# Performance work log

Measured on AMD Instinct MI355X. Metric: run time of the kernel, lower is better.

## Reference

```python
import jax, jax.numpy as jnp
import numpy as np

B, SQ, SKV, D = 4, 2048, 2048, 1024
HEADS, DIM_HEAD = 16, 64
SCALE = DIM_HEAD ** -0.5


def setup_inputs() -> dict:
    key = jax.random.key(0)
    ks = jax.random.split(key, 7)
    s = 0.02  # keep pre-softmax logits in a sane range
    return {
        "hidden_states": jax.random.normal(ks[0], (B, SQ, D), dtype=jnp.float32),
        "encoder_hidden_states": jax.random.normal(ks[1], (B, SKV, D), dtype=jnp.float32),
        "Wq": jax.random.normal(ks[2], (D, D), dtype=jnp.float32) * s,
        "Wk": jax.random.normal(ks[3], (D, D), dtype=jnp.float32) * s,
        "Wv": jax.random.normal(ks[4], (D, D), dtype=jnp.float32) * s,
        "Wo": jax.random.normal(ks[5], (D, D), dtype=jnp.float32) * s,
        "bo": jnp.zeros((D,), dtype=jnp.float32),
    }


def reference(hidden_states, encoder_hidden_states, Wq, Wk, Wv, Wo, bo):
    # to_q / to_k / to_v (bias=False)
    q = hidden_states @ Wq                       # [B, SQ, H*Dh]
    k = encoder_hidden_states @ Wk               # [B, SKV, H*Dh]
    v = encoder_hidden_states @ Wv
    # head split: [B, S, H, Dh]
    q = q.reshape(B, SQ, HEADS, DIM_HEAD)
    k = k.reshape(B, SKV, HEADS, DIM_HEAD)
    v = v.reshape(B, SKV, HEADS, DIM_HEAD)
    # scaled QK^T (baddbmm with beta=0, alpha=scale), softmax over keys
    scores = jnp.einsum("bqhd,bkhd->bhqk", q, k) * SCALE  # [B, H, SQ, SKV]
    probs = jax.nn.softmax(scores, axis=-1)
    # attention-weighted values, merge heads
    out = jnp.einsum("bhqk,bkhd->bqhd", probs, v).reshape(B, SQ, HEADS * DIM_HEAD)
    # to_out[0] linear (with bias); to_out[1] Dropout(0.0) is identity
    return out @ Wo + bo
```

## Files before the change

kernel.cpp:

```cpp
#include <hip/hip_runtime.h>

#define BATCH 4
#define SQ 2048
#define SKV 2048
#define DMODEL 1024
#define HEADS 16
#define DH 64

typedef __bf16 bf8_t __attribute__((ext_vector_type(8)));
typedef float f4_t __attribute__((ext_vector_type(4)));
typedef float f16_t __attribute__((ext_vector_type(16)));
typedef unsigned int u32;
typedef unsigned short ush;

static __device__ __forceinline__ ush f2bf(float f) {
  __bf16 h = (__bf16)f;
  return __builtin_bit_cast(ush, h);
}
static __device__ __forceinline__ u32 pk2(float a, float b) {
  return (u32)f2bf(a) | ((u32)f2bf(b) << 16);
}
static __device__ __forceinline__ void async16(const ush* g, ush* l) {
  __builtin_amdgcn_global_load_lds((const __attribute__((address_space(1))) unsigned int*)g,
                                   (__attribute__((address_space(3))) unsigned int*)l, 16, 0, 0);
}
static __device__ __forceinline__ void barrier_f() {
  asm volatile("" ::: "memory");
  __builtin_amdgcn_s_barrier();
  asm volatile("" ::: "memory");
}

__global__ __launch_bounds__(256) void prep_k(const float* __restrict__ hs,
                                              const float* __restrict__ ehs,
                                              const float* __restrict__ W0,
                                              const float* __restrict__ W1,
                                              const float* __restrict__ W2,
                                              const float* __restrict__ W3,
                                              ush* __restrict__ wT,
                                              ush* __restrict__ hsb, ush* __restrict__ ehsb) {
  __shared__ ush t[64][72];
  const int bx = blockIdx.x;
  const int tid = threadIdx.x;
  if (bx < 8192) {
    const float* X = bx < 4096 ? hs : ehs;
    ush* Y = bx < 4096 ? hsb : ehsb;
    const size_t i = ((size_t)(bx & 4095) * 256 + tid) * 8;
    float4 a = *reinterpret_cast<const float4*>(X + i);
    float4 b = *reinterpret_cast<const float4*>(X + i + 4);
    uint4 u = {pk2(a.x, a.y), pk2(a.z, a.w), pk2(b.x, b.y), pk2(b.z, b.w)};
    *reinterpret_cast<uint4*>(Y + i) = u;
    return;
  }
  const int idx = bx - 8192;
  const int z = idx >> 8, kb = (idx >> 4) & 15, nb = idx & 15;
  const float* W = z == 0 ? W0 : z == 1 ? W1 : z == 2 ? W2 : W3;
  const float scl = (z == 0) ? 0.125f * 1.44269504088896f : 1.0f;
  ush* o = wT + (size_t)z * (DMODEL * DMODEL);
  const int k0 = kb * 64, n0 = nb * 64;
#pragma unroll
  for (int it = 0; it < 4; ++it) {
    int c = tid + it * 256;
    int r = c >> 4, q4 = c & 15;
    float4 v = *reinterpret_cast<const float4*>(&W[(size_t)(k0 + r) * DMODEL + n0 + q4 * 4]);
    t[q4 * 4 + 0][r] = f2bf(v.x * scl);
    t[q4 * 4 + 1][r] = f2bf(v.y * scl);
    t[q4 * 4 + 2][r] = f2bf(v.z * scl);
    t[q4 * 4 + 3][r] = f2bf(v.w * scl);
  }
  __syncthreads();
#pragma unroll
  for (int it = 0; it < 2; ++it) {
    int c = tid + it * 256;
    int r = c >> 3, s8 = c & 7;
    uint4 pv;
    pv.x = (u32)t[r][s8 * 8 + 0] | ((u32)t[r][s8 * 8 + 1] << 16);
    pv.y = (u32)t[r][s8 * 8 + 2] | ((u32)t[r][s8 * 8 + 3] << 16);
    pv.z = (u32)t[r][s8 * 8 + 4] | ((u32)t[r][s8 * 8 + 5] << 16);
    pv.w = (u32)t[r][s8 * 8 + 6] | ((u32)t[r][s8 * 8 + 7] << 16);
    *reinterpret_cast<uint4*>(&o[(size_t)(n0 + r) * DMODEL + k0 + s8 * 8]) = pv;
  }
}

__global__ __launch_bounds__(256, 2) void proj_k(const ush* __restrict__ hsb,
                                                 const ush* __restrict__ ehsb,
                                                 const ush* __restrict__ AO,
                                                 const ush* __restrict__ wT,
                                                 ush* __restrict__ Qb, ush* __restrict__ K2,
                                                 ush* __restrict__ V2, float* __restrict__ out,
                                                 const float* __restrict__ bias, int segbase) {
  __shared__ ush As[2][128 * 64];
  __shared__ ush Bs[2][128 * 64];
  const int tid = threadIdx.x;
  const int lane = tid & 63, w = tid >> 6;
  const int wr = w >> 1, wc = w & 1;
  const int lr = lane & 15, lg = lane >> 4;
  const int bid = blockIdx.x;
  const int seg = segbase + (bid >> 9);
  const int t = bid & 511;
  const int m0 = (t >> 3) * 128, n0 = (t & 7) * 128;
  const ush* A = seg == 0 ? hsb : (seg == 3 ? AO : ehsb);
  const ush* BT = wT + (size_t)seg * (DMODEL * DMODEL);

  auto stage = [&](int bf, int kt) {
    const int kb = kt * 64;
#pragma unroll
    for (int ch = 0; ch < 4; ++ch) {
      const int g = ch * 256 + tid;
      const int r = g >> 3, s8 = (g & 7) ^ (r & 7);
      async16(A + (size_t)(m0 + r) * DMODEL + kb + s8 * 8, &As[bf][(ch * 256 + w * 64) * 8]);
      async16(BT + (size_t)(n0 + r) * DMODEL + kb + s8 * 8, &Bs[bf][(ch * 256 + w * 64) * 8]);
    }
  };

  f4_t acc[4][4] = {};
  stage(0, 0);
  for (int kt = 0; kt < DMODEL / 64; ++kt) {
    const int cur = kt & 1;
    barrier_f();
    if (kt + 1 < DMODEL / 64) {
      stage(cur ^ 1, kt + 1);
      asm volatile("s_waitcnt vmcnt(8)" ::: "memory");
    } else {
      asm volatile("s_waitcnt vmcnt(0)" ::: "memory");
    }
    barrier_f();
#pragma unroll
    for (int ks = 0; ks < 2; ++ks) {
      bf8_t a[4], b[4];
#pragma unroll
      for (int rf = 0; rf < 4; ++rf) {
        const int row = wr * 64 + rf * 16 + lr;
        a[rf] = *reinterpret_cast<const bf8_t*>(
            &As[cur][(row * 64 + ks * 32 + lg * 8) ^ ((row & 7) << 3)]);
      }
#pragma unroll
      for (int cf = 0; cf < 4; ++cf) {
        const int nn = wc * 64 + cf * 16 + lr;
        b[cf] = *reinterpret_cast<const bf8_t*>(
            &Bs[cur][(nn * 64 + ks * 32 + lg * 8) ^ ((nn & 7) << 3)]);
      }
      __builtin_amdgcn_s_setprio(1);
#pragma unroll
      for (int rf = 0; rf < 4; ++rf)
#pragma unroll
        for (int cf = 0; cf < 4; ++cf)
          acc[rf][cf] = __builtin_amdgcn_mfma_f32_16x16x32_bf16(a[rf], b[cf], acc[rf][cf], 0, 0, 0);
      __builtin_amdgcn_s_setprio(0);
    }
  }
  if (seg == 1) {
#pragma unroll
    for (int rf = 0; rf < 4; ++rf)
#pragma unroll
      for (int cf = 0; cf < 4; ++cf) {
        const int n = n0 + wc * 64 + cf * 16 + lr;
        const int h = n >> 6, dd = n & 63;
        const int fd = dd >> 4, hi2 = (dd >> 3) & 1, e = dd & 7;
#pragma unroll
        for (int i = 0; i < 4; ++i) {
          const int row = m0 + wr * 64 + rf * 16 + lg * 4 + i;
          const int bb = row >> 11, s = row & 2047;
          const int kt = s >> 6, kvi = s & 63;
          const size_t addr =
              ((((size_t)(bb * 16 + h) * 32 + kt) * 8 + fd * 2 + hi2) * 64 + kvi) * 8 + e;
          K2[addr] = f2bf(acc[rf][cf][i]);
        }
      }
  } else if (seg == 2) {
#pragma unroll
    for (int rf = 0; rf < 4; ++rf)
#pragma unroll
      for (int cf = 0; cf < 4; ++cf) {
        const int row0 = m0 + wr * 64 + rf * 16 + lg * 4;
        const int bb = row0 >> 11, s0 = row0 & 2047;
        const int kt = s0 >> 6, ks = (s0 >> 4) & 3, hi2 = (s0 >> 3) & 1, e0 = s0 & 7;
        const int n = n0 + wc * 64 + cf * 16 + lr;
        const int h = n >> 6, dd = n & 63;
        ushort4 u;
        u.x = f2bf(acc[rf][cf][0]);
        u.y = f2bf(acc[rf][cf][1]);
        u.z = f2bf(acc[rf][cf][2]);
        u.w = f2bf(acc[rf][cf][3]);
        const size_t addr =
            ((((size_t)(bb * 16 + h) * 32 + kt) * 8 + ks * 2 + hi2) * 64 + dd) * 8 + e0;
        *reinterpret_cast<ushort4*>(&V2[addr]) = u;
      }
  } else if (seg == 3) {
#pragma unroll
    for (int cf = 0; cf < 4; ++cf) {
      const int col = n0 + wc * 64 + cf * 16 + lr;
      const float bv = bias[col];
#pragma unroll
      for (int rf = 0; rf < 4; ++rf)
#pragma unroll
        for (int i = 0; i < 4; ++i) {
          const int row = m0 + wr * 64 + rf * 16 + lg * 4 + i;
          out[(size_t)row * DMODEL + col] = acc[rf][cf][i] + bv;
        }
    }
  } else {
#pragma unroll
    for (int rf = 0; rf < 4; ++rf)
#pragma unroll
      for (int cf = 0; cf < 4; ++cf)
#pragma unroll
        for (int i = 0; i < 4; ++i) {
          const int row = m0 + wr * 64 + rf * 16 + lg * 4 + i;
          const int col = n0 + wc * 64 + cf * 16 + lr;
          Qb[(size_t)row * DMODEL + col] = f2bf(acc[rf][cf][i]);
        }
  }
}

__global__ __launch_bounds__(256, 4) void attn_k(const ush* __restrict__ Qb,
                                                 const ush* __restrict__ K2,
                                                 const ush* __restrict__ V2,
                                                 ush* __restrict__ AO) {
  __shared__ ush Ks[2][4096];
  __shared__ ush Vs[2][4096];
  const int tid = threadIdx.x;
  const int lane = tid & 63, w = tid >> 6;
  const int rw = lane & 31, hi = lane >> 5;

  const int bid = blockIdx.x;
  const int swz = (bid & 7) * 128 + (bid >> 3);
  const int hl = swz >> 4;
  const int qb = swz & 15;
  const int b = hl >> 4, h = hl & 15;
  const int q0 = qb * 128 + w * 32;

  const ush* Qp = Qb + ((size_t)(b * SQ + q0 + rw)) * DMODEL + h * DH + hi * 8;
  bf8_t qf[4];
#pragma unroll
  for (int f = 0; f < 4; ++f) qf[f] = *reinterpret_cast<const bf8_t*>(Qp + 16 * f);

  bf8_t ones;
#pragma unroll
  for (int i = 0; i < 8; ++i) ones[i] = __builtin_bit_cast(__bf16, (ush)0x3F80);

  f16_t acc0 = {}, acc1 = {}, sacc = {};

  const ush* Kh = K2 + (size_t)hl * 131072;
  const ush* Vh = V2 + (size_t)hl * 131072;

  auto stage = [&](int bf, int kt) {
    const ush* ksrc = Kh + (size_t)kt * 4096;
    const ush* vsrc = Vh + (size_t)kt * 4096;
#pragma unroll
    for (int ch = 0; ch < 2; ++ch) {
      const int off = (ch * 256 + tid) * 8;
      async16(ksrc + off, &Ks[bf][(ch * 256 + w * 64) * 8]);
      async16(vsrc + off, &Vs[bf][(ch * 256 + w * 64) * 8]);
    }
  };

  stage(0, 0);
  int cur = 0;
  for (int kt = 0; kt < SKV / 64; ++kt) {
    barrier_f();
    if (kt + 1 < SKV / 64) {
      stage(cur ^ 1, kt + 1);
      asm volatile("s_waitcnt vmcnt(4)" ::: "memory");
    } else {
      asm volatile("s_waitcnt vmcnt(0)" ::: "memory");
    }
    barrier_f();

    f16_t s0 = {}, s1 = {};
    __builtin_amdgcn_s_setprio(1);
#pragma unroll
    for (int f = 0; f < 4; ++f) {
      const int base = (f * 128 + hi * 64 + rw) * 8;
      bf8_t k0 = *reinterpret_cast<const bf8_t*>(&Ks[cur][base]);
      bf8_t k1 = *reinterpret_cast<const bf8_t*>(&Ks[cur][base + 256]);
      s0 = __builtin_amdgcn_mfma_f32_32x32x16_bf16(k0, qf[f], s0, 0, 0, 0);
      s1 = __builtin_amdgcn_mfma_f32_32x32x16_bf16(k1, qf[f], s1, 0, 0, 0);
    }
    __builtin_amdgcn_s_setprio(0);

#pragma unroll
    for (int i = 0; i < 16; ++i) s0[i] = __builtin_amdgcn_exp2f(s0[i]);
#pragma unroll
    for (int i = 0; i < 16; ++i) s1[i] = __builtin_amdgcn_exp2f(s1[i]);

    __builtin_amdgcn_s_setprio(1);
#pragma unroll
    for (int kb = 0; kb < 2; ++kb) {
      const f16_t& sv = kb ? s1 : s0;
      bf8_t pf[2];
      {
        u32 w0 = pk2(sv[0], sv[1]), w2 = pk2(sv[4], sv[5]);
        asm volatile("v_permlane32_swap_b32 %0, %1" : "+v"(w0), "+v"(w2));
        u32 w1 = pk2(sv[2], sv[3]), w3 = pk2(sv[6], sv[7]);
        asm volatile("v_permlane32_swap_b32 %0, %1" : "+v"(w1), "+v"(w3));
        uint4 t0 = {w0, w1, w2, w3};
        pf[0] = __builtin_bit_cast(bf8_t, t0);
        u32 x0 = pk2(sv[8], sv[9]), x2 = pk2(sv[12], sv[13]);
        asm volatile("v_permlane32_swap_b32 %0, %1" : "+v"(x0), "+v"(x2));
        u32 x1 = pk2(sv[10], sv[11]), x3 = pk2(sv[14], sv[15]);
        asm volatile("v_permlane32_swap_b32 %0, %1" : "+v"(x1), "+v"(x3));
        uint4 t1 = {x0, x1, x2, x3};
        pf[1] = __builtin_bit_cast(bf8_t, t1);
      }
#pragma unroll
      for (int s = 0; s < 2; ++s) {
        const int vbase = ((2 * kb + s) * 128 + hi * 64 + rw) * 8;
        bf8_t v0 = *reinterpret_cast<const bf8_t*>(&Vs[cur][vbase]);
        bf8_t v1 = *reinterpret_cast<const bf8_t*>(&Vs[cur][vbase + 256]);
        acc0 = __builtin_amdgcn_mfma_f32_32x32x16_bf16(v0, pf[s], acc0, 0, 0, 0);
        acc1 = __builtin_amdgcn_mfma_f32_32x32x16_bf16(v1, pf[s], acc1, 0, 0, 0);
        sacc = __builtin_amdgcn_mfma_f32_32x32x16_bf16(ones, pf[s], sacc, 0, 0, 0);
      }
    }
    __builtin_amdgcn_s_setprio(0);
    cur ^= 1;
  }

  const float inv = 1.f / sacc[0];
  ush* Op = AO + ((size_t)(b * SQ + q0 + rw)) * DMODEL + h * DH;
#pragma unroll
  for (int db = 0; db < 2; ++db) {
    const f16_t& A = db ? acc1 : acc0;
#pragma unroll
    for (int r = 0; r < 16; r += 2) {
      const int d = db * 32 + (r & 3) + 8 * (r >> 2) + 4 * hi;
      *reinterpret_cast<u32*>(Op + d) = pk2(A[r] * inv, A[r + 1] * inv);
    }
  }
}

extern "C" void kernel_launch(void* const* d_in, const int* in_sizes, int n_in,
                              void* d_out, int out_size, void* d_ws, size_t ws_size,
                              hipStream_t stream) {
  const float* hs = (const float*)d_in[0];
  const float* ehs = (const float*)d_in[1];
  const float* Wq = (const float*)d_in[2];
  const float* Wk = (const float*)d_in[3];
  const float* Wv = (const float*)d_in[4];
  const float* Wo = (const float*)d_in[5];
  const float* bo = (const float*)d_in[6];
  float* out = (float*)d_out;

  unsigned short* ws = (unsigned short*)d_ws;
  const size_t MM = (size_t)1024 * 1024;
  unsigned short* wT = ws;
  unsigned short* Qb = ws + 4 * MM;
  unsigned short* K2 = Qb + 8 * MM;
  unsigned short* V2 = K2 + 8 * MM;
  unsigned short* AO = V2 + 8 * MM;
  unsigned short* hsb = (unsigned short*)d_out;
  unsigned short* ehsb = hsb + 8 * MM;

  prep_k<<<dim3(9216), 256, 0, stream>>>(hs, ehs, Wq, Wk, Wv, Wo, wT, hsb, ehsb);
  proj_k<<<dim3(1536), 256, 0, stream>>>(hsb, ehsb, AO, wT, Qb, K2, V2, out, bo, 0);
  attn_k<<<dim3(1024), 256, 0, stream>>>(Qb, K2, V2, AO);
  proj_k<<<dim3(512), 256, 0, stream>>>(hsb, ehsb, AO, wT, Qb, K2, V2, out, bo, 3);
}
```

Before: 204.4 us.

## Software-pipeline attention loop so PV of previous tile overlaps QK of current

Restructures the attention inner loop: the QK^T MFMAs for tile kt are issued together with the PV MFMAs for tile kt-1, and the exp/pack of the new scores follows. This lets the matrix unit keep working while the exp and permlane packing run, instead of serialising QK, exp, then PV. V tiles move to a triple buffer so the previous tile's V stays resident while the next one loads. The cost is extra LDS (a third V buffer), a prologue and epilogue, and more live registers for the packed P fragments, which may pressure occupancy at launch bounds of 4.

```diff
diff --git a/kernel.cpp b/kernel.cpp
--- a/kernel.cpp
+++ b/kernel.cpp
@@ -217,7 +217,7 @@
                                                  const ush* __restrict__ V2,
                                                  ush* __restrict__ AO) {
   __shared__ ush Ks[2][4096];
-  __shared__ ush Vs[2][4096];
+  __shared__ ush Vs[3][4096];
   const int tid = threadIdx.x;
   const int lane = tid & 63, w = tid >> 6;
   const int rw = lane & 31, hi = lane >> 5;
@@ -239,27 +239,70 @@
   for (int i = 0; i < 8; ++i) ones[i] = __builtin_bit_cast(__bf16, (ush)0x3F80);
 
   f16_t acc0 = {}, acc1 = {}, sacc = {};
+  bf8_t pf[4];
 
   const ush* Kh = K2 + (size_t)hl * 131072;
   const ush* Vh = V2 + (size_t)hl * 131072;
 
-  auto stage = [&](int bf, int kt) {
+  auto stage = [&](int kbf, int vbf, int kt) {
     const ush* ksrc = Kh + (size_t)kt * 4096;
     const ush* vsrc = Vh + (size_t)kt * 4096;
 #pragma unroll
     for (int ch = 0; ch < 2; ++ch) {
       const int off = (ch * 256 + tid) * 8;
-      async16(ksrc + off, &Ks[bf][(ch * 256 + w * 64) * 8]);
-      async16(vsrc + off, &Vs[bf][(ch * 256 + w * 64) * 8]);
+      async16(ksrc + off, &Ks[kbf][(ch * 256 + w * 64) * 8]);
+      async16(vsrc + off, &Vs[vbf][(ch * 256 + w * 64) * 8]);
     }
   };
 
-  stage(0, 0);
-  int cur = 0;
-  for (int kt = 0; kt < SKV / 64; ++kt) {
+  auto packP = [&](const f16_t& s0, const f16_t& s1) {
+#pragma unroll
+    for (int kb = 0; kb < 2; ++kb) {
+      const f16_t& sv = kb ? s1 : s0;
+      u32 w0 = pk2(sv[0], sv[1]), w2 = pk2(sv[4], sv[5]);
+      asm volatile("v_permlane32_swap_b32 %0, %1" : "+v"(w0), "+v"(w2));
+      u32 w1 = pk2(sv[2], sv[3]), w3 = pk2(sv[6], sv[7]);
+      asm volatile("v_permlane32_swap_b32 %0, %1" : "+v"(w1), "+v"(w3));
+      uint4 t0 = {w0, w1, w2, w3};
+      pf[kb * 2 + 0] = __builtin_bit_cast(bf8_t, t0);
+      u32 x0 = pk2(sv[8], sv[9]), x2 = pk2(sv[12], sv[13]);
+      asm volatile("v_permlane32_swap_b32 %0, %1" : "+v"(x0), "+v"(x2));
+      u32 x1 = pk2(sv[10], sv[11]), x3 = pk2(sv[14], sv[15]);
+      asm volatile("v_permlane32_swap_b32 %0, %1" : "+v"(x1), "+v"(x3));
+      uint4 t1 = {x0, x1, x2, x3};
+      pf[kb * 2 + 1] = __builtin_bit_cast(bf8_t, t1);
+    }
+  };
+
+  stage(0, 0, 0);
+  stage(1, 1, 1);
+  asm volatile("s_waitcnt vmcnt(4)" ::: "memory");
+  barrier_f();
+  {
+    f16_t s0 = {}, s1 = {};
+    __builtin_amdgcn_s_setprio(1);
+#pragma unroll
+    for (int f = 0; f < 4; ++f) {
+      const int base = (f * 128 + hi * 64 + rw) * 8;
+      bf8_t k0 = *reinterpret_cast<const bf8_t*>(&Ks[0][base]);
+      bf8_t k1 = *reinterpret_cast<const bf8_t*>(&Ks[0][base + 256]);
+      s0 = __builtin_amdgcn_mfma_f32_32x32x16_bf16(k0, qf[f], s0, 0, 0, 0);
+      s1 = __builtin_amdgcn_mfma_f32_32x32x16_bf16(k1, qf[f], s1, 0, 0, 0);
+    }
+    __builtin_amdgcn_s_setprio(0);
+#pragma unroll
+    for (int i = 0; i < 16; ++i) s0[i] = __builtin_amdgcn_exp2f(s0[i]);
+#pragma unroll
+    for (int i = 0; i < 16; ++i) s1[i] = __builtin_amdgcn_exp2f(s1[i]);
+    packP(s0, s1);
+  }
+
+  for (int kt = 1; kt < SKV / 64; ++kt) {
+    const int cur = kt & 1;
+    const int vprev = (kt - 1) % 3;
     barrier_f();
     if (kt + 1 < SKV / 64) {
-      stage(cur ^ 1, kt + 1);
+      stage(cur ^ 1, (kt + 1) % 3, kt + 1);
       asm volatile("s_waitcnt vmcnt(4)" ::: "memory");
     } else {
       asm volatile("s_waitcnt vmcnt(0)" ::: "memory");
@@ -276,44 +319,37 @@
       s0 = __builtin_amdgcn_mfma_f32_32x32x16_bf16(k0, qf[f], s0, 0, 0, 0);
       s1 = __builtin_amdgcn_mfma_f32_32x32x16_bf16(k1, qf[f], s1, 0, 0, 0);
     }
+#pragma unroll
+    for (int s = 0; s < 4; ++s) {
+      const int vbase = (s * 128 + hi * 64 + rw) * 8;
+      bf8_t v0 = *reinterpret_cast<const bf8_t*>(&Vs[vprev][vbase]);
+      bf8_t v1 = *reinterpret_cast<const bf8_t*>(&Vs[vprev][vbase + 256]);
+      acc0 = __builtin_amdgcn_mfma_f32_32x32x16_bf16(v0, pf[s], acc0, 0, 0, 0);
+      acc1 = __builtin_amdgcn_mfma_f32_32x32x16_bf16(v1, pf[s], acc1, 0, 0, 0);
+      sacc = __builtin_amdgcn_mfma_f32_32x32x16_bf16(ones, pf[s], sacc, 0, 0, 0);
+    }
     __builtin_amdgcn_s_setprio(0);
 
 #pragma unroll
     for (int i = 0; i < 16; ++i) s0[i] = __builtin_amdgcn_exp2f(s0[i]);
 #pragma unroll
     for (int i = 0; i < 16; ++i) s1[i] = __builtin_amdgcn_exp2f(s1[i]);
-
+    packP(s0, s1);
+  }
+
+  {
+    const int vprev = (SKV / 64 - 1) % 3;
     __builtin_amdgcn_s_setprio(1);
 #pragma unroll
-    for (int kb = 0; kb < 2; ++kb) {
-      const f16_t& sv = kb ? s1 : s0;
-      bf8_t pf[2];
-      {
-        u32 w0 = pk2(sv[0], sv[1]), w2 = pk2(sv[4], sv[5]);
-        asm volatile("v_permlane32_swap_b32 %0, %1" : "+v"(w0), "+v"(w2));
-        u32 w1 = pk2(sv[2], sv[3]), w3 = pk2(sv[6], sv[7]);
-        asm volatile("v_permlane32_swap_b32 %0, %1" : "+v"(w1), "+v"(w3));
-        uint4 t0 = {w0, w1, w2, w3};
-        pf[0] = __builtin_bit_cast(bf8_t, t0);
-        u32 x0 = pk2(sv[8], sv[9]), x2 = pk2(sv[12], sv[13]);
-        asm volatile("v_permlane32_swap_b32 %0, %1" : "+v"(x0), "+v"(x2));
-        u32 x1 = pk2(sv[10], sv[11]), x3 = pk2(sv[14], sv[15]);
-        asm volatile("v_permlane32_swap_b32 %0, %1" : "+v"(x1), "+v"(x3));
-        uint4 t1 = {x0, x1, x2, x3};
-        pf[1] = __builtin_bit_cast(bf8_t, t1);
-      }
-#pragma unroll
-      for (int s = 0; s < 2; ++s) {
-        const int vbase = ((2 * kb + s) * 128 + hi * 64 + rw) * 8;
-        bf8_t v0 = *reinterpret_cast<const bf8_t*>(&Vs[cur][vbase]);
-        bf8_t v1 = *reinterpret_cast<const bf8_t*>(&Vs[cur][vbase + 256]);
-        acc0 = __builtin_amdgcn_mfma_f32_32x32x16_bf16(v0, pf[s], acc0, 0, 0, 0);
-        acc1 = __builtin_amdgcn_mfma_f32_32x32x16_bf16(v1, pf[s], acc1, 0, 0, 0);
-        sacc = __builtin_amdgcn_mfma_f32_32x32x16_bf16(ones, pf[s], sacc, 0, 0, 0);
-      }
+    for (int s = 0; s < 4; ++s) {
+      const int vbase = (s * 128 + hi * 64 + rw) * 8;
+      bf8_t v0 = *reinterpret_cast<const bf8_t*>(&Vs[vprev][vbase]);
+      bf8_t v1 = *reinterpret_cast<const bf8_t*>(&Vs[vprev][vbase + 256]);
+      acc0 = __builtin_amdgcn_mfma_f32_32x32x16_bf16(v0, pf[s], acc0, 0, 0, 0);
+      acc1 = __builtin_amdgcn_mfma_f32_32x32x16_bf16(v1, pf[s], acc1, 0, 0, 0);
+      sacc = __builtin_amdgcn_mfma_f32_32x32x16_bf16(ones, pf[s], sacc, 0, 0, 0);
     }
     __builtin_amdgcn_s_setprio(0);
-    cur ^= 1;
   }
 
   const float inv = 1.f / sacc[0];
```

Measured after the change: 322.9 us. 57.9% more time.

## Add 256x256-tile 512-thread QKV projection kernel with interleaved prefetch

Applied to the files above, without the earlier changes.

Adds a dedicated QKV projection kernel using 256x256 output tiles with 8 waves per block, so each loaded A/B tile feeds more MFMA work. The next k-tile's async global-to-LDS loads are spread across the four MFMA sub-phases instead of issued in one burst. Grid tiles are swizzled across blocks, and the old kernel keeps only the output-projection epilogue. The larger tiles use 128KB of LDS and more accumulator registers per thread, and give only 384 blocks, which risks lower occupancy and uneven work across CUs.

```diff
diff --git a/kernel.cpp b/kernel.cpp
--- a/kernel.cpp
+++ b/kernel.cpp
@@ -81,6 +81,138 @@
   }
 }
 
+__global__ __launch_bounds__(512, 2) void proj8_k(const ush* __restrict__ hsb,
+                                                  const ush* __restrict__ ehsb,
+                                                  const ush* __restrict__ wT,
+                                                  ush* __restrict__ Qb, ush* __restrict__ K2,
+                                                  ush* __restrict__ V2) {
+  __shared__ ush As[2][16384];
+  __shared__ ush Bs[2][16384];
+  const int tid = threadIdx.x;
+  const int lane = tid & 63, w = tid >> 6;
+  const int wr = w >> 2, wc = w & 3;
+  const int lr = lane & 15, lg = lane >> 4;
+
+  const int bid = blockIdx.x;
+  const int swz = (bid & 7) * 48 + (bid >> 3);
+  const int seg = swz >> 7;
+  const int t = swz & 127;
+  const int m0 = (t >> 2) * 256, n0 = (t & 3) * 256;
+  const ush* A = (seg == 0) ? hsb : ehsb;
+  const ush* BT = wT + (size_t)seg * (DMODEL * DMODEL);
+
+  const int srow = tid >> 3;
+  const int s8 = (tid & 7) ^ (srow & 7);
+  auto stage_round = [&](int bf, int kt, int r) {
+    const ush* src = (r < 4) ? A + (size_t)(m0 + r * 64 + srow) * DMODEL + kt * 64 + s8 * 8
+                             : BT + (size_t)(n0 + (r - 4) * 64 + srow) * DMODEL + kt * 64 + s8 * 8;
+    ush* dst = (r < 4 ? As[bf] : Bs[bf]) + (r & 3) * 4096 + w * 512;
+    async16(src, dst);
+  };
+
+  f4_t acc[8][4] = {};
+
+#pragma unroll
+  for (int r = 0; r < 8; ++r) stage_round(0, 0, r);
+  asm volatile("s_waitcnt vmcnt(0)" ::: "memory");
+  barrier_f();
+
+  for (int kt = 0; kt < DMODEL / 64; ++kt) {
+    const int cur = kt & 1;
+    bf8_t bfr[4][2];
+#pragma unroll
+    for (int pp = 0; pp < 4; ++pp) {
+      if (pp == 0) {
+#pragma unroll
+        for (int nf = 0; nf < 4; ++nf)
+#pragma unroll
+          for (int ks = 0; ks < 2; ++ks) {
+            const int rr = wc * 64 + nf * 16 + lr;
+            bfr[nf][ks] = *reinterpret_cast<const bf8_t*>(
+                &Bs[cur][(rr * 64 + ks * 32 + lg * 8) ^ ((rr & 7) << 3)]);
+          }
+      }
+      bf8_t afr[2][2];
+#pragma unroll
+      for (int mf = 0; mf < 2; ++mf)
+#pragma unroll
+        for (int ks = 0; ks < 2; ++ks) {
+          const int rr = wr * 128 + (2 * pp + mf) * 16 + lr;
+          afr[mf][ks] = *reinterpret_cast<const bf8_t*>(
+              &As[cur][(rr * 64 + ks * 32 + lg * 8) ^ ((rr & 7) << 3)]);
+        }
+      if (kt + 1 < DMODEL / 64) {
+        stage_round(cur ^ 1, kt + 1, 2 * pp);
+        stage_round(cur ^ 1, kt + 1, 2 * pp + 1);
+      }
+      __builtin_amdgcn_s_setprio(1);
+#pragma unroll
+      for (int mf = 0; mf < 2; ++mf)
+#pragma unroll
+        for (int nf = 0; nf < 4; ++nf)
+#pragma unroll
+          for (int ks = 0; ks < 2; ++ks)
+            acc[2 * pp + mf][nf] = __builtin_amdgcn_mfma_f32_16x16x32_bf16(
+                afr[mf][ks], bfr[nf][ks], acc[2 * pp + mf][nf], 0, 0, 0);
+      __builtin_amdgcn_s_setprio(0);
+    }
+    if (kt + 1 < DMODEL / 64) {
+      asm volatile("s_waitcnt vmcnt(0)" ::: "memory");
+    }
+    barrier_f();
+  }
+
+  if (seg == 0) {
+#pragma unroll
+    for (int m = 0; m < 8; ++m)
+#pragma unroll
+      for (int nf = 0; nf < 4; ++nf)
+#pragma unroll
+        for (int i = 0; i < 4; ++i) {
+          const int row = m0 + wr * 128 + m * 16 + lg * 4 + i;
+          const int col = n0 + wc * 64 + nf * 16 + lr;
+          Qb[(size_t)row * DMODEL + col] = f2bf(acc[m][nf][i]);
+        }
+  } else if (seg == 1) {
+#pragma unroll
+    for (int m = 0; m < 8; ++m)
+#pragma unroll
+      for (int nf = 0; nf < 4; ++nf) {
+        const int n = n0 + wc * 64 + nf * 16 + lr;
+        const int h = n >> 6, dd = n & 63;
+        const int fd = dd >> 4, hi2 = (dd >> 3) & 1, e = dd & 7;
+#pragma unroll
+        for (int i = 0; i < 4; ++i) {
+          const int row = m0 + wr * 128 + m * 16 + lg * 4 + i;
+          const int bb = row >> 11, s = row & 2047;
+          const int kti = s >> 6, kvi = s & 63;
+          const size_t addr =
+              ((((size_t)(bb * 16 + h) * 32 + kti) * 8 + fd * 2 + hi2) * 64 + kvi) * 8 + e;
+          K2[addr] = f2bf(acc[m][nf][i]);
+        }
+      }
+  } else {
+#pragma unroll
+    for (int m = 0; m < 8; ++m)
+#pragma unroll
+      for (int nf = 0; nf < 4; ++nf) {
+        const int row0 = m0 + wr * 128 + m * 16 + lg * 4;
+        const int bb = row0 >> 11, s0 = row0 & 2047;
+        const int kti = s0 >> 6, ks2 = (s0 >> 4) & 3, hi2 = (s0 >> 3) & 1, e0 = s0 & 7;
+        const int n = n0 + wc * 64 + nf * 16 + lr;
+        const int h = n >> 6, dd = n & 63;
+        ushort4 u;
+        u.x = f2bf(acc[m][nf][0]);
+        u.y = f2bf(acc[m][nf][1]);
+        u.z = f2bf(acc[m][nf][2]);
+        u.w = f2bf(acc[m][nf][3]);
+        const size_t addr =
+            ((((size_t)(bb * 16 + h) * 32 + kti) * 8 + ks2 * 2 + hi2) * 64 + dd) * 8 + e0;
+        *reinterpret_cast<ushort4*>(&V2[addr]) = u;
+      }
+  }
+}
+
 __global__ __launch_bounds__(256, 2) void proj_k(const ush* __restrict__ hsb,
                                                  const ush* __restrict__ ehsb,
                                                  const ush* __restrict__ AO,
@@ -148,44 +280,7 @@
       __builtin_amdgcn_s_setprio(0);
     }
   }
-  if (seg == 1) {
-#pragma unroll
-    for (int rf = 0; rf < 4; ++rf)
-#pragma unroll
-      for (int cf = 0; cf < 4; ++cf) {
-        const int n = n0 + wc * 64 + cf * 16 + lr;
-        const int h = n >> 6, dd = n & 63;
-        const int fd = dd >> 4, hi2 = (dd >> 3) & 1, e = dd & 7;
-#pragma unroll
-        for (int i = 0; i < 4; ++i) {
-          const int row = m0 + wr * 64 + rf * 16 + lg * 4 + i;
-          const int bb = row >> 11, s = row & 2047;
-          const int kt = s >> 6, kvi = s & 63;
-          const size_t addr =
-              ((((size_t)(bb * 16 + h) * 32 + kt) * 8 + fd * 2 + hi2) * 64 + kvi) * 8 + e;
-          K2[addr] = f2bf(acc[rf][cf][i]);
-        }
-      }
-  } else if (seg == 2) {
-#pragma unroll
-    for (int rf = 0; rf < 4; ++rf)
-#pragma unroll
-      for (int cf = 0; cf < 4; ++cf) {
-        const int row0 = m0 + wr * 64 + rf * 16 + lg * 4;
-        const int bb = row0 >> 11, s0 = row0 & 2047;
-        const int kt = s0 >> 6, ks = (s0 >> 4) & 3, hi2 = (s0 >> 3) & 1, e0 = s0 & 7;
-        const int n = n0 + wc * 64 + cf * 16 + lr;
-        const int h = n >> 6, dd = n & 63;
-        ushort4 u;
-        u.x = f2bf(acc[rf][cf][0]);
-        u.y = f2bf(acc[rf][cf][1]);
-        u.z = f2bf(acc[rf][cf][2]);
-        u.w = f2bf(acc[rf][cf][3]);
-        const size_t addr =
-            ((((size_t)(bb * 16 + h) * 32 + kt) * 8 + ks * 2 + hi2) * 64 + dd) * 8 + e0;
-        *reinterpret_cast<ushort4*>(&V2[addr]) = u;
-      }
-  } else if (seg == 3) {
+  if (seg == 3) {
 #pragma unroll
     for (int cf = 0; cf < 4; ++cf) {
       const int col = n0 + wc * 64 + cf * 16 + lr;
@@ -198,17 +293,6 @@
           out[(size_t)row * DMODEL + col] = acc[rf][cf][i] + bv;
         }
     }
-  } else {
-#pragma unroll
-    for (int rf = 0; rf < 4; ++rf)
-#pragma unroll
-      for (int cf = 0; cf < 4; ++cf)
-#pragma unroll
-        for (int i = 0; i < 4; ++i) {
-          const int row = m0 + wr * 64 + rf * 16 + lg * 4 + i;
-          const int col = n0 + wc * 64 + cf * 16 + lr;
-          Qb[(size_t)row * DMODEL + col] = f2bf(acc[rf][cf][i]);
-        }
   }
 }
 
@@ -352,7 +436,7 @@
   unsigned short* ehsb = hsb + 8 * MM;
 
   prep_k<<<dim3(9216), 256, 0, stream>>>(hs, ehs, Wq, Wk, Wv, Wo, wT, hsb, ehsb);
-  proj_k<<<dim3(1536), 256, 0, stream>>>(hsb, ehsb, AO, wT, Qb, K2, V2, out, bo, 0);
+  proj8_k<<<dim3(384), 512, 0, stream>>>(hsb, ehsb, wT, Qb, K2, V2);
   attn_k<<<dim3(1024), 256, 0, stream>>>(Qb, K2, V2, AO);
   proj_k<<<dim3(512), 256, 0, stream>>>(hsb, ehsb, AO, wT, Qb, K2, V2, out, bo, 3);
 }
```

Result: no change. 207.0 us (+1.2%).

## Process two 32-row query chunks per wave and sum softmax denominators in VALU

Applied to the files above, without the earlier changes.

Each wave now handles 64 query rows instead of 32, so every K/V tile staged in LDS is reused across twice as many queries, and the grid is halved. The row-sum of probabilities is no longer computed with an extra MFMA against a ones vector; it is accumulated with VALU adds and combined across half-waves with a shuffle. Register pressure roughly doubles, so launch bounds drop to 2 blocks per SM, which lowers occupancy and latency hiding.

```diff
diff --git a/kernel.cpp b/kernel.cpp
--- a/kernel.cpp
+++ b/kernel.cpp
@@ -212,7 +212,7 @@
   }
 }
 
-__global__ __launch_bounds__(256, 4) void attn_k(const ush* __restrict__ Qb,
+__global__ __launch_bounds__(256, 2) void attn_k(const ush* __restrict__ Qb,
                                                  const ush* __restrict__ K2,
                                                  const ush* __restrict__ V2,
                                                  ush* __restrict__ AO) {
@@ -223,22 +223,22 @@
   const int rw = lane & 31, hi = lane >> 5;
 
   const int bid = blockIdx.x;
-  const int swz = (bid & 7) * 128 + (bid >> 3);
-  const int hl = swz >> 4;
-  const int qb = swz & 15;
+  const int swz = (bid & 7) * 64 + (bid >> 3);
+  const int hl = swz >> 3;
+  const int qb = swz & 7;
   const int b = hl >> 4, h = hl & 15;
-  const int q0 = qb * 128 + w * 32;
-
-  const ush* Qp = Qb + ((size_t)(b * SQ + q0 + rw)) * DMODEL + h * DH + hi * 8;
-  bf8_t qf[4];
-#pragma unroll
-  for (int f = 0; f < 4; ++f) qf[f] = *reinterpret_cast<const bf8_t*>(Qp + 16 * f);
-
-  bf8_t ones;
-#pragma unroll
-  for (int i = 0; i < 8; ++i) ones[i] = __builtin_bit_cast(__bf16, (ush)0x3F80);
-
-  f16_t acc0 = {}, acc1 = {}, sacc = {};
+  const int q0 = qb * 256 + w * 64;
+
+  bf8_t qf[2][4];
+#pragma unroll
+  for (int c = 0; c < 2; ++c) {
+    const ush* Qp = Qb + ((size_t)(b * SQ + q0 + c * 32 + rw)) * DMODEL + h * DH + hi * 8;
+#pragma unroll
+    for (int f = 0; f < 4; ++f) qf[c][f] = *reinterpret_cast<const bf8_t*>(Qp + 16 * f);
+  }
+
+  f16_t acc00 = {}, acc01 = {}, acc10 = {}, acc11 = {};
+  float lsum0 = 0.f, lsum1 = 0.f;
 
   const ush* Kh = K2 + (size_t)hl * 131072;
   const ush* Vh = V2 + (size_t)hl * 131072;
@@ -266,65 +266,108 @@
     }
     barrier_f();
 
-    f16_t s0 = {}, s1 = {};
+    f16_t s00 = {}, s01 = {}, s10 = {}, s11 = {};
     __builtin_amdgcn_s_setprio(1);
 #pragma unroll
     for (int f = 0; f < 4; ++f) {
       const int base = (f * 128 + hi * 64 + rw) * 8;
       bf8_t k0 = *reinterpret_cast<const bf8_t*>(&Ks[cur][base]);
       bf8_t k1 = *reinterpret_cast<const bf8_t*>(&Ks[cur][base + 256]);
-      s0 = __builtin_amdgcn_mfma_f32_32x32x16_bf16(k0, qf[f], s0, 0, 0, 0);
-      s1 = __builtin_amdgcn_mfma_f32_32x32x16_bf16(k1, qf[f], s1, 0, 0, 0);
+      s00 = __builtin_amdgcn_mfma_f32_32x32x16_bf16(k0, qf[0][f], s00, 0, 0, 0);
+      s01 = __builtin_amdgcn_mfma_f32_32x32x16_bf16(k1, qf[0][f], s01, 0, 0, 0);
+      s10 = __builtin_amdgcn_mfma_f32_32x32x16_bf16(k0, qf[1][f], s10, 0, 0, 0);
+      s11 = __builtin_amdgcn_mfma_f32_32x32x16_bf16(k1, qf[1][f], s11, 0, 0, 0);
     }
     __builtin_amdgcn_s_setprio(0);
 
 #pragma unroll
-    for (int i = 0; i < 16; ++i) s0[i] = __builtin_amdgcn_exp2f(s0[i]);
-#pragma unroll
-    for (int i = 0; i < 16; ++i) s1[i] = __builtin_amdgcn_exp2f(s1[i]);
-
-    __builtin_amdgcn_s_setprio(1);
-#pragma unroll
-    for (int kb = 0; kb < 2; ++kb) {
-      const f16_t& sv = kb ? s1 : s0;
-      bf8_t pf[2];
-      {
+    for (int i = 0; i < 16; ++i) s00[i] = __builtin_amdgcn_exp2f(s00[i]);
+#pragma unroll
+    for (int i = 0; i < 16; ++i) s01[i] = __builtin_amdgcn_exp2f(s01[i]);
+#pragma unroll
+    for (int i = 0; i < 16; ++i) s10[i] = __builtin_amdgcn_exp2f(s10[i]);
+#pragma unroll
+    for (int i = 0; i < 16; ++i) s11[i] = __builtin_amdgcn_exp2f(s11[i]);
+    {
+      float t0 = 0.f, t1 = 0.f, t2 = 0.f, t3 = 0.f;
+#pragma unroll
+      for (int i = 0; i < 16; i += 4) {
+        t0 += s00[i];
+        t1 += s00[i + 1];
+        t2 += s00[i + 2];
+        t3 += s00[i + 3];
+        t0 += s01[i];
+        t1 += s01[i + 1];
+        t2 += s01[i + 2];
+        t3 += s01[i + 3];
+      }
+      lsum0 += (t0 + t1) + (t2 + t3);
+    }
+    {
+      float t0 = 0.f, t1 = 0.f, t2 = 0.f, t3 = 0.f;
+#pragma unroll
+      for (int i = 0; i < 16; i += 4) {
+        t0 += s10[i];
+        t1 += s10[i + 1];
+        t2 += s10[i + 2];
+        t3 += s10[i + 3];
+        t0 += s11[i];
+        t1 += s11[i + 1];
+        t2 += s11[i + 2];
+        t3 += s11[i + 3];
+      }
+      lsum1 += (t0 + t1) + (t2 + t3);
+    }
+
+    bf8_t pf[2][4];
+#pragma unroll
+    for (int cb = 0; cb < 2; ++cb)
+#pragma unroll
+      for (int kb = 0; kb < 2; ++kb) {
+        const f16_t& sv = cb ? (kb ? s11 : s10) : (kb ? s01 : s00);
         u32 w0 = pk2(sv[0], sv[1]), w2 = pk2(sv[4], sv[5]);
         asm volatile("v_permlane32_swap_b32 %0, %1" : "+v"(w0), "+v"(w2));
         u32 w1 = pk2(sv[2], sv[3]), w3 = pk2(sv[6], sv[7]);
         asm volatile("v_permlane32_swap_b32 %0, %1" : "+v"(w1), "+v"(w3));
         uint4 t0 = {w0, w1, w2, w3};
-        pf[0] = __builtin_bit_cast(bf8_t, t0);
+        pf[cb][kb * 2 + 0] = __builtin_bit_cast(bf8_t, t0);
         u32 x0 = pk2(sv[8], sv[9]), x2 = pk2(sv[12], sv[13]);
         asm volatile("v_permlane32_swap_b32 %0, %1" : "+v"(x0), "+v"(x2));
         u32 x1 = pk2(sv[10], sv[11]), x3 = pk2(sv[14], sv[15]);
         asm volatile("v_permlane32_swap_b32 %0, %1" : "+v"(x1), "+v"(x3));
         uint4 t1 = {x0, x1, x2, x3};
-        pf[1] = __builtin_bit_cast(bf8_t, t1);
-      }
-#pragma unroll
-      for (int s = 0; s < 2; ++s) {
-        const int vbase = ((2 * kb + s) * 128 + hi * 64 + rw) * 8;
-        bf8_t v0 = *reinterpret_cast<const bf8_t*>(&Vs[cur][vbase]);
-        bf8_t v1 = *reinterpret_cast<const bf8_t*>(&Vs[cur][vbase + 256]);
-        acc0 = __builtin_amdgcn_mfma_f32_32x32x16_bf16(v0, pf[s], acc0, 0, 0, 0);
-        acc1 = __builtin_amdgcn_mfma_f32_32x32x16_bf16(v1, pf[s], acc1, 0, 0, 0);
-        sacc = __builtin_amdgcn_mfma_f32_32x32x16_bf16(ones, pf[s], sacc, 0, 0, 0);
-      }
+        pf[cb][kb * 2 + 1] = __builtin_bit_cast(bf8_t, t1);
+      }
+
+    __builtin_amdgcn_s_setprio(1);
+#pragma unroll
+    for (int ks = 0; ks < 4; ++ks) {
+      const int vbase = (ks * 128 + hi * 64 + rw) * 8;
+      bf8_t v0 = *reinterpret_cast<const bf8_t*>(&Vs[cur][vbase]);
+      bf8_t v1 = *reinterpret_cast<const bf8_t*>(&Vs[cur][vbase + 256]);
+      acc00 = __builtin_amdgcn_mfma_f32_32x32x16_bf16(v0, pf[0][ks], acc00, 0, 0, 0);
+      acc01 = __builtin_amdgcn_mfma_f32_32x32x16_bf16(v1, pf[0][ks], acc01, 0, 0, 0);
+      acc10 = __builtin_amdgcn_mfma_f32_32x32x16_bf16(v0, pf[1][ks], acc10, 0, 0, 0);
+      acc11 = __builtin_amdgcn_mfma_f32_32x32x16_bf16(v1, pf[1][ks], acc11, 0, 0, 0);
     }
     __builtin_amdgcn_s_setprio(0);
     cur ^= 1;
   }
 
-  const float inv = 1.f / sacc[0];
-  ush* Op = AO + ((size_t)(b * SQ + q0 + rw)) * DMODEL + h * DH;
-#pragma unroll
-  for (int db = 0; db < 2; ++db) {
-    const f16_t& A = db ? acc1 : acc0;
-#pragma unroll
-    for (int r = 0; r < 16; r += 2) {
-      const int d = db * 32 + (r & 3) + 8 * (r >> 2) + 4 * hi;
-      *reinterpret_cast<u32*>(Op + d) = pk2(A[r] * inv, A[r + 1] * inv);
+#pragma unroll
+  for (int cb = 0; cb < 2; ++cb) {
+    float ls = cb ? lsum1 : lsum0;
+    const float lrow = ls + __shfl_xor(ls, 32, 64);
+    const float inv = 1.f / lrow;
+    ush* Op = AO + ((size_t)(b * SQ + q0 + cb * 32 + rw)) * DMODEL + h * DH;
+#pragma unroll
+    for (int db = 0; db < 2; ++db) {
+      const f16_t& A = db ? (cb ? acc11 : acc01) : (cb ? acc10 : acc00);
+#pragma unroll
+      for (int r = 0; r < 16; r += 2) {
+        const int d = db * 32 + (r & 3) + 8 * (r >> 2) + 4 * hi;
+        *reinterpret_cast<u32*>(Op + d) = pk2(A[r] * inv, A[r + 1] * inv);
+      }
     }
   }
 }
@@ -353,6 +396,6 @@
 
   prep_k<<<dim3(9216), 256, 0, stream>>>(hs, ehs, Wq, Wk, Wv, Wo, wT, hsb, ehsb);
   proj_k<<<dim3(1536), 256, 0, stream>>>(hsb, ehsb, AO, wT, Qb, K2, V2, out, bo, 0);
-  attn_k<<<dim3(1024), 256, 0, stream>>>(Qb, K2, V2, AO);
+  attn_k<<<dim3(512), 256, 0, stream>>>(Qb, K2, V2, AO);
   proj_k<<<dim3(512), 256, 0, stream>>>(hsb, ehsb, AO, wT, Qb, K2, V2, out, bo, 3);
 }
```

Result: no change. 202.4 us (-1.0%).
